# Performance work log

Measured on AMD Instinct MI355X. Metric: run time of the kernel, lower is better.

## Reference

```python
import jax, jax.numpy as jnp
import numpy as np

EMBED_DIM = 512
FFN_DIM = 64
N_QUBITS = 16
BATCH = 16
SEQ = 4096


def setup_inputs() -> dict:
    key = jax.random.key(0)
    ks = jax.random.split(key, 6)
    x = jax.random.normal(ks[0], (BATCH, SEQ, EMBED_DIM), dtype=jnp.float32)
    theta = jax.random.normal(ks[1], (N_QUBITS,), dtype=jnp.float32)
    W1 = jax.random.normal(ks[2], (FFN_DIM, N_QUBITS), dtype=jnp.float32) * (1.0 / np.sqrt(N_QUBITS))
    b1 = jax.random.normal(ks[3], (FFN_DIM,), dtype=jnp.float32) * 0.02
    W2 = jax.random.normal(ks[4], (EMBED_DIM, FFN_DIM), dtype=jnp.float32) * (1.0 / np.sqrt(FFN_DIM))
    b2 = jax.random.normal(ks[5], (EMBED_DIM,), dtype=jnp.float32) * 0.02
    return {"x": x, "theta": theta, "W1": W1, "b1": b1, "W2": W2, "b2": b2}


def reference(x, theta, W1, b1, W2, b2):
    # Quantum circuit closed form: per wire i, |0> -> RX(x_i) -> RY(theta_i),
    # <PauliZ> = cos(x_i) * cos(theta_i). Only the first n_qubits features of x are encoded.
    z = jnp.cos(x[..., :N_QUBITS]) * jnp.cos(theta)              # [B, S, Q]
    h = jnp.einsum('bsq,fq->bsf', z, W1) + b1                    # [B, S, F] (dropout is identity at eval)
    out = jnp.einsum('bsf,ef->bse', jax.nn.relu(h), W2) + b2     # [B, S, E]
    return out
```

## Files before the change

kernel.cpp:

```cpp
#include <hip/hip_runtime.h>
#include <hip/hip_bf16.h>


#define EMBED 512
#define FFN   64
#define NQ    16
#define ROWS  65536
#define ROWS_PER_BLOCK 128
#define MITERS (ROWS_PER_BLOCK / 16)
#define NBLOCKS (ROWS / ROWS_PER_BLOCK)

typedef __attribute__((ext_vector_type(8))) short short8;
typedef __attribute__((ext_vector_type(4))) short short4_t;
typedef __attribute__((ext_vector_type(4))) float floatx4;

__device__ __forceinline__ short f2bf(float f) {
    union { float f; unsigned u; } v; v.f = f;
    unsigned u = v.u;
    unsigned r = (u + 0x7fffu + ((u >> 16) & 1u)) >> 16;
    return (short)r;
}

__global__ __launch_bounds__(256, 2)
void ffq_kernel(const float* __restrict__ x,
                const float* __restrict__ theta,
                const float* __restrict__ W1,
                const float* __restrict__ b1,
                const float* __restrict__ W2,
                const float* __restrict__ b2,
                float* __restrict__ out)
{
    __shared__ __align__(16) float w1_s[FFN][NQ];
    __shared__ __align__(16) float z_s[2][16][20];
    __shared__ __align__(16) short h_s[2][16][72];

    const int t    = threadIdx.x;
    const int lane = t & 63;
    const int w    = t >> 6;
    const int quad = lane >> 4;
    const int l16  = lane & 15;

    ((float4*)&w1_s[0][0])[t] = ((const float4*)W1)[t];

    const float cth = cosf(theta[t & 15]);
    const float4 b1v = ((const float4*)b1)[t >> 4];
    float b1a[4] = {b1v.x, b1v.y, b1v.z, b1v.w};

    float b2r[8];
#pragma unroll
    for (int tile = 0; tile < 8; ++tile)
        b2r[tile] = b2[w * 128 + tile * 16 + l16];

    short8 bfrag[8][2];
#pragma unroll
    for (int tile = 0; tile < 8; ++tile) {
        const int e = w * 128 + tile * 16 + l16;
#pragma unroll
        for (int s = 0; s < 2; ++s) {
            const int f0 = s * 32 + quad * 8;
            const float4* p = (const float4*)(W2 + (size_t)e * FFN + f0);
            float4 lo = p[0], hi = p[1];
            short8 bfr;
            bfr[0] = f2bf(lo.x); bfr[1] = f2bf(lo.y); bfr[2] = f2bf(lo.z); bfr[3] = f2bf(lo.w);
            bfr[4] = f2bf(hi.x); bfr[5] = f2bf(hi.y); bfr[6] = f2bf(hi.z); bfr[7] = f2bf(hi.w);
            bfrag[tile][s] = bfr;
        }
    }

    const int rowBase = blockIdx.x * ROWS_PER_BLOCK;

    for (int it = 0; it < MITERS; ++it) {
        const int buf  = it & 1;
        const int row0 = rowBase + it * 16;

        {
            const int zr = t >> 4, zq = t & 15;
            const float xv = x[(size_t)(row0 + zr) * EMBED + zq];
            z_s[buf][zr][zq] = cosf(xv) * cth;
        }
        __syncthreads();

        {
            const int r = t & 15, g = t >> 4;
            const float4 zr0 = *(const float4*)&z_s[buf][r][0];
            const float4 zr1 = *(const float4*)&z_s[buf][r][4];
            const float4 zr2 = *(const float4*)&z_s[buf][r][8];
            const float4 zr3 = *(const float4*)&z_s[buf][r][12];
            short4_t hv;
#pragma unroll
            for (int i = 0; i < 4; ++i) {
                const float4* wr = (const float4*)&w1_s[g * 4 + i][0];
                const float4 w0 = wr[0], w1r = wr[1], w2r = wr[2], w3r = wr[3];
                float s0 = b1a[i];
                s0 += zr0.x * w0.x  + zr0.y * w0.y  + zr0.z * w0.z  + zr0.w * w0.w;
                s0 += zr1.x * w1r.x + zr1.y * w1r.y + zr1.z * w1r.z + zr1.w * w1r.w;
                s0 += zr2.x * w2r.x + zr2.y * w2r.y + zr2.z * w2r.z + zr2.w * w2r.w;
                s0 += zr3.x * w3r.x + zr3.y * w3r.y + zr3.z * w3r.z + zr3.w * w3r.w;
                s0 = fmaxf(s0, 0.0f);
                hv[i] = f2bf(s0);
            }
            *(short4_t*)&h_s[buf][r][g * 4] = hv;
        }
        __syncthreads();

        const short8 a0 = *(const short8*)&h_s[buf][l16][quad * 8];
        const short8 a1 = *(const short8*)&h_s[buf][l16][32 + quad * 8];

#pragma unroll
        for (int tile = 0; tile < 8; ++tile) {
            floatx4 acc = {0.f, 0.f, 0.f, 0.f};
            acc = __builtin_amdgcn_mfma_f32_16x16x32_bf16(a0, bfrag[tile][0], acc, 0, 0, 0);
            acc = __builtin_amdgcn_mfma_f32_16x16x32_bf16(a1, bfrag[tile][1], acc, 0, 0, 0);

            const int e = w * 128 + tile * 16 + l16;
#pragma unroll
            for (int reg = 0; reg < 4; ++reg) {
                const int r = row0 + quad * 4 + reg;
                out[(size_t)r * EMBED + e] = acc[reg] + b2r[tile];
            }
        }
    }
}

extern "C" void kernel_launch(void* const* d_in, const int* in_sizes, int n_in,
                              void* d_out, int out_size, void* d_ws, size_t ws_size,
                              hipStream_t stream) {
    const float* x     = (const float*)d_in[0];
    const float* theta = (const float*)d_in[1];
    const float* W1    = (const float*)d_in[2];
    const float* b1    = (const float*)d_in[3];
    const float* W2    = (const float*)d_in[4];
    const float* b2    = (const float*)d_in[5];
    float* out = (float*)d_out;

    ffq_kernel<<<NBLOCKS, 256, 0, stream>>>(x, theta, W1, b1, W2, b2, out);
}
```

Measured before the change: 226.7 us.

## Compute first FFN layer with MFMA in registers, drop shared memory and barriers

Moves the first projection (z·W1ᵀ + b1) onto MFMA. cos(theta) is folded into W1 fragments and the layer-1 accumulator layout is chosen so it feeds the layer-2 A operand directly, which removes shared-memory staging and both __syncthreads per iteration. It also cuts rows per block from 128 to 32 for more blocks, switches to fast __cosf, and folds b2 into the MFMA accumulator init. In exchange, each block now recomputes the W2 and W1 fragments over fewer rows, and z is rounded to bf16 with a lower-accuracy cosine.

```diff
diff --git a/kernel.cpp b/kernel.cpp
--- a/kernel.cpp
+++ b/kernel.cpp
@@ -4,14 +4,11 @@
 
 #define EMBED 512
 #define FFN   64
-#define NQ    16
 #define ROWS  65536
-#define ROWS_PER_BLOCK 128
-#define MITERS (ROWS_PER_BLOCK / 16)
+#define ROWS_PER_BLOCK 32
 #define NBLOCKS (ROWS / ROWS_PER_BLOCK)
 
 typedef __attribute__((ext_vector_type(8))) short short8;
-typedef __attribute__((ext_vector_type(4))) short short4_t;
 typedef __attribute__((ext_vector_type(4))) float floatx4;
 
 __device__ __forceinline__ short f2bf(float f) {
@@ -19,6 +16,13 @@
     unsigned u = v.u;
     unsigned r = (u + 0x7fffu + ((u >> 16) & 1u)) >> 16;
     return (short)r;
+}
+
+__device__ __forceinline__ short8 pack8(float4 a, float4 b) {
+    short8 r;
+    r[0] = f2bf(a.x); r[1] = f2bf(a.y); r[2] = f2bf(a.z); r[3] = f2bf(a.w);
+    r[4] = f2bf(b.x); r[5] = f2bf(b.y); r[6] = f2bf(b.z); r[7] = f2bf(b.w);
+    return r;
 }
 
 __global__ __launch_bounds__(256, 2)
@@ -30,94 +34,93 @@
                 const float* __restrict__ b2,
                 float* __restrict__ out)
 {
-    __shared__ __align__(16) float w1_s[FFN][NQ];
-    __shared__ __align__(16) float z_s[2][16][20];
-    __shared__ __align__(16) short h_s[2][16][72];
+    const int t     = threadIdx.x;
+    const int lane  = t & 63;
+    const int w     = t >> 6;
+    const int quad  = lane >> 4;
+    const int l16   = lane & 15;
+    const int ebase = w * 128;
 
-    const int t    = threadIdx.x;
-    const int lane = t & 63;
-    const int w    = t >> 6;
-    const int quad = lane >> 4;
-    const int l16  = lane & 15;
+    short8 a1frag[4];
+#pragma unroll
+    for (int tf = 0; tf < 4; ++tf) a1frag[tf] = (short8){0,0,0,0,0,0,0,0};
+    if (quad < 2) {
+        float ct[8];
+#pragma unroll
+        for (int j = 0; j < 8; ++j) ct[j] = __cosf(theta[quad * 8 + j]);
+#pragma unroll
+        for (int tf = 0; tf < 4; ++tf) {
+            const float4* wp = (const float4*)(W1 + (size_t)(16 * tf + l16) * 16 + quad * 8);
+            float4 wa = wp[0], wb = wp[1];
+            float4 pa, pb;
+            pa.x = wa.x * ct[0]; pa.y = wa.y * ct[1]; pa.z = wa.z * ct[2]; pa.w = wa.w * ct[3];
+            pb.x = wb.x * ct[4]; pb.y = wb.y * ct[5]; pb.z = wb.z * ct[6]; pb.w = wb.w * ct[7];
+            a1frag[tf] = pack8(pa, pb);
+        }
+    }
 
-    ((float4*)&w1_s[0][0])[t] = ((const float4*)W1)[t];
-
-    const float cth = cosf(theta[t & 15]);
-    const float4 b1v = ((const float4*)b1)[t >> 4];
-    float b1a[4] = {b1v.x, b1v.y, b1v.z, b1v.w};
+    floatx4 b1c[4];
+#pragma unroll
+    for (int tf = 0; tf < 4; ++tf) {
+        float4 v = *(const float4*)(b1 + 16 * tf + quad * 4);
+        b1c[tf] = (floatx4){v.x, v.y, v.z, v.w};
+    }
 
     float b2r[8];
 #pragma unroll
-    for (int tile = 0; tile < 8; ++tile)
-        b2r[tile] = b2[w * 128 + tile * 16 + l16];
+    for (int te = 0; te < 8; ++te)
+        b2r[te] = b2[ebase + te * 16 + l16];
 
     short8 bfrag[8][2];
 #pragma unroll
-    for (int tile = 0; tile < 8; ++tile) {
-        const int e = w * 128 + tile * 16 + l16;
-#pragma unroll
-        for (int s = 0; s < 2; ++s) {
-            const int f0 = s * 32 + quad * 8;
-            const float4* p = (const float4*)(W2 + (size_t)e * FFN + f0);
-            float4 lo = p[0], hi = p[1];
-            short8 bfr;
-            bfr[0] = f2bf(lo.x); bfr[1] = f2bf(lo.y); bfr[2] = f2bf(lo.z); bfr[3] = f2bf(lo.w);
-            bfr[4] = f2bf(hi.x); bfr[5] = f2bf(hi.y); bfr[6] = f2bf(hi.z); bfr[7] = f2bf(hi.w);
-            bfrag[tile][s] = bfr;
-        }
+    for (int te = 0; te < 8; ++te) {
+        const float* wrow = W2 + (size_t)(ebase + te * 16 + l16) * FFN;
+        float4 g0 = *(const float4*)(wrow +  0 + quad * 4);
+        float4 g1 = *(const float4*)(wrow + 16 + quad * 4);
+        float4 g2 = *(const float4*)(wrow + 32 + quad * 4);
+        float4 g3 = *(const float4*)(wrow + 48 + quad * 4);
+        bfrag[te][0] = pack8(g0, g1);
+        bfrag[te][1] = pack8(g2, g3);
     }
 
     const int rowBase = blockIdx.x * ROWS_PER_BLOCK;
 
-    for (int it = 0; it < MITERS; ++it) {
-        const int buf  = it & 1;
+#pragma unroll
+    for (int it = 0; it < 2; ++it) {
         const int row0 = rowBase + it * 16;
 
-        {
-            const int zr = t >> 4, zq = t & 15;
-            const float xv = x[(size_t)(row0 + zr) * EMBED + zq];
-            z_s[buf][zr][zq] = cosf(xv) * cth;
+        short8 zf = (short8){0,0,0,0,0,0,0,0};
+        if (quad < 2) {
+            const float4* xr = (const float4*)(x + (size_t)(row0 + l16) * EMBED + quad * 8);
+            float4 xa = xr[0], xb = xr[1];
+            float4 ca, cb;
+            ca.x = __cosf(xa.x); ca.y = __cosf(xa.y); ca.z = __cosf(xa.z); ca.w = __cosf(xa.w);
+            cb.x = __cosf(xb.x); cb.y = __cosf(xb.y); cb.z = __cosf(xb.z); cb.w = __cosf(xb.w);
+            zf = pack8(ca, cb);
         }
-        __syncthreads();
 
-        {
-            const int r = t & 15, g = t >> 4;
-            const float4 zr0 = *(const float4*)&z_s[buf][r][0];
-            const float4 zr1 = *(const float4*)&z_s[buf][r][4];
-            const float4 zr2 = *(const float4*)&z_s[buf][r][8];
-            const float4 zr3 = *(const float4*)&z_s[buf][r][12];
-            short4_t hv;
+        floatx4 acc1[4];
 #pragma unroll
-            for (int i = 0; i < 4; ++i) {
-                const float4* wr = (const float4*)&w1_s[g * 4 + i][0];
-                const float4 w0 = wr[0], w1r = wr[1], w2r = wr[2], w3r = wr[3];
-                float s0 = b1a[i];
-                s0 += zr0.x * w0.x  + zr0.y * w0.y  + zr0.z * w0.z  + zr0.w * w0.w;
-                s0 += zr1.x * w1r.x + zr1.y * w1r.y + zr1.z * w1r.z + zr1.w * w1r.w;
-                s0 += zr2.x * w2r.x + zr2.y * w2r.y + zr2.z * w2r.z + zr2.w * w2r.w;
-                s0 += zr3.x * w3r.x + zr3.y * w3r.y + zr3.z * w3r.z + zr3.w * w3r.w;
-                s0 = fmaxf(s0, 0.0f);
-                hv[i] = f2bf(s0);
-            }
-            *(short4_t*)&h_s[buf][r][g * 4] = hv;
+        for (int tf = 0; tf < 4; ++tf)
+            acc1[tf] = __builtin_amdgcn_mfma_f32_16x16x32_bf16(a1frag[tf], zf, b1c[tf], 0, 0, 0);
+
+        short8 a20, a21;
+#pragma unroll
+        for (int j = 0; j < 8; ++j) {
+            a20[j] = f2bf(fmaxf(acc1[(j >> 2)][j & 3], 0.0f));
+            a21[j] = f2bf(fmaxf(acc1[2 + (j >> 2)][j & 3], 0.0f));
         }
-        __syncthreads();
-
-        const short8 a0 = *(const short8*)&h_s[buf][l16][quad * 8];
-        const short8 a1 = *(const short8*)&h_s[buf][l16][32 + quad * 8];
 
 #pragma unroll
-        for (int tile = 0; tile < 8; ++tile) {
-            floatx4 acc = {0.f, 0.f, 0.f, 0.f};
-            acc = __builtin_amdgcn_mfma_f32_16x16x32_bf16(a0, bfrag[tile][0], acc, 0, 0, 0);
-            acc = __builtin_amdgcn_mfma_f32_16x16x32_bf16(a1, bfrag[tile][1], acc, 0, 0, 0);
+        for (int te = 0; te < 8; ++te) {
+            floatx4 c = (floatx4){b2r[te], b2r[te], b2r[te], b2r[te]};
+            c = __builtin_amdgcn_mfma_f32_16x16x32_bf16(a20, bfrag[te][0], c, 0, 0, 0);
+            c = __builtin_amdgcn_mfma_f32_16x16x32_bf16(a21, bfrag[te][1], c, 0, 0, 0);
 
-            const int e = w * 128 + tile * 16 + l16;
+            float* po = out + (size_t)(row0 + quad * 4) * EMBED + ebase + te * 16 + l16;
 #pragma unroll
-            for (int reg = 0; reg < 4; ++reg) {
-                const int r = row0 + quad * 4 + reg;
-                out[(size_t)r * EMBED + e] = acc[reg] + b2r[tile];
-            }
+            for (int reg = 0; reg < 4; ++reg)
+                po[(size_t)reg * EMBED] = c[reg];
         }
     }
 }
```

Result: slower. 242.1 us (+6.8%).
